# Kernel tuning notes

Hardware: AMD Instinct MI355X
Metric: run time of the kernel (lower is better)

## Reference

```python
import jax, jax.numpy as jnp
import numpy as np


def setup_inputs() -> dict:
    key = jax.random.key(0)
    ks = jax.random.split(key, 4)
    B, H, W, C = 4, 64, 64, 256
    d = C // 8
    x = jax.random.normal(ks[0], (B, H, W, C), dtype=jnp.float32)
    # 1x1 conv weights as [C_in, C_out] matrices (Glorot-ish scale)
    Wq = jax.random.normal(ks[1], (C, d), dtype=jnp.float32) * (1.0 / np.sqrt(C))
    Wk = jax.random.normal(ks[2], (C, d), dtype=jnp.float32) * (1.0 / np.sqrt(C))
    Wv = jax.random.normal(ks[3], (C, C), dtype=jnp.float32) * (1.0 / np.sqrt(C))
    bq = jnp.zeros((d,), dtype=jnp.float32)
    bk = jnp.zeros((d,), dtype=jnp.float32)
    bv = jnp.zeros((C,), dtype=jnp.float32)
    gamma = jnp.float32(0.0)  # matches tf.Variable(0.0)
    return {"x": x, "Wq": Wq, "bq": bq, "Wk": Wk, "bk": bk, "Wv": Wv, "bv": bv, "gamma": gamma}


def reference(x, Wq, bq, Wk, bk, Wv, bv, gamma):
    B, H, W, C = x.shape
    N = H * W
    xf = x.reshape(B, N, C)  # spatial tokens
    q = xf @ Wq + bq  # [B, N, d]
    k = xf @ Wk + bk  # [B, N, d]
    v = xf @ Wv + bv  # [B, N, C]
    energy = jnp.einsum("bnd,bmd->bnm", q, k)  # [B, N, N]
    attn = jax.nn.softmax(energy, axis=-1)
    out = jnp.einsum("bnm,bmc->bnc", attn, v).reshape(B, H, W, C)
    return gamma * out + x
```

## Files before the change

### kernel.cpp

```cpp
#include <hip/hip_runtime.h>
#include <hip/hip_bf16.h>

typedef __attribute__((ext_vector_type(8)))  short short8;
typedef __attribute__((ext_vector_type(4)))  float f32x4;
typedef __attribute__((ext_vector_type(16))) float f32x16;
typedef __attribute__((ext_vector_type(4)))  unsigned int u32x4;

#define LOG2E 1.4426950408889634f

static __device__ __forceinline__ unsigned short f2bf(float f) {
    union { float f; unsigned u; } v; v.f = f;
    unsigned r = v.u + 0x7fffu + ((v.u >> 16) & 1u);
    return (unsigned short)(r >> 16);
}
static __device__ __forceinline__ unsigned cvt_pk_bf16(float lo, float hi) {
    unsigned r;
    asm("v_cvt_pk_bf16_f32 %0, %1, %2" : "=v"(r) : "v"(lo), "v"(hi));
    return r;
}
static __device__ __forceinline__ float exp2_hw(float x) {
    float r;
    asm("v_exp_f32 %0, %1" : "=v"(r) : "v"(x));
    return r;
}

__global__ __launch_bounds__(64) void transpose_w(
    const float* __restrict__ Wq, const float* __restrict__ Wk,
    const float* __restrict__ Wv, unsigned short* __restrict__ Wtf)
{
    const int g  = blockIdx.x;
    const int ct = g >> 3, kk = g & 7;
    const int l  = threadIdx.x;
    const int col = ct * 16 + (l & 15);
    const int k0  = kk * 32 + (l >> 4) * 8;
    const float* W; int c, ldw;
    if (col < 32)      { W = Wq; c = col;      ldw = 32;  }
    else if (col < 64) { W = Wk; c = col - 32; ldw = 32;  }
    else               { W = Wv; c = col - 64; ldw = 256; }
    ushort4 o0, o1;
    o0.x = f2bf(W[(size_t)(k0 + 0) * ldw + c]);
    o0.y = f2bf(W[(size_t)(k0 + 1) * ldw + c]);
    o0.z = f2bf(W[(size_t)(k0 + 2) * ldw + c]);
    o0.w = f2bf(W[(size_t)(k0 + 3) * ldw + c]);
    o1.x = f2bf(W[(size_t)(k0 + 4) * ldw + c]);
    o1.y = f2bf(W[(size_t)(k0 + 5) * ldw + c]);
    o1.z = f2bf(W[(size_t)(k0 + 6) * ldw + c]);
    o1.w = f2bf(W[(size_t)(k0 + 7) * ldw + c]);
    *reinterpret_cast<ushort4*>(Wtf + (size_t)g * 512 + l * 8)     = o0;
    *reinterpret_cast<ushort4*>(Wtf + (size_t)g * 512 + l * 8 + 4) = o1;
}

__global__ __launch_bounds__(256) void proj_kernel(
    const float* __restrict__ x, const unsigned short* __restrict__ Wtf,
    const float* __restrict__ bq, const float* __restrict__ bk,
    const float* __restrict__ bv,
    unsigned short* __restrict__ Qb, unsigned short* __restrict__ Kf,
    unsigned short* __restrict__ Vf)
{
    __shared__ unsigned short x_lds[64][264];
    const int tid = threadIdx.x;
    const int M0  = (blockIdx.x >> 1) * 64;
    const int ctb = (blockIdx.x & 1) * 10;

    #pragma unroll
    for (int j = 0; j < 16; ++j) {
        int idx = j * 256 + tid;
        int row = idx >> 6;
        int qc  = idx & 63;
        const float4 v = *reinterpret_cast<const float4*>(x + (size_t)(M0 + row) * 256 + qc * 4);
        ushort4 o;
        o.x = f2bf(v.x); o.y = f2bf(v.y); o.z = f2bf(v.z); o.w = f2bf(v.w);
        *reinterpret_cast<ushort4*>(&x_lds[row][qc * 4]) = o;
    }
    __syncthreads();

    const int w  = tid >> 6;
    const int l  = tid & 63;
    const int lr = l & 15;
    const int lg = l >> 4;

    short8 a[8];
    #pragma unroll
    for (int kk = 0; kk < 8; ++kk)
        a[kk] = *reinterpret_cast<const short8*>(&x_lds[w * 16 + lr][kk * 32 + lg * 8]);

    const int b   = M0 >> 12;
    const int kt  = (M0 & 4095) >> 6;

    for (int ct = ctb; ct < ctb + 10; ++ct) {
        const int col = ct * 16 + lr;
        f32x4 acc = {0.f, 0.f, 0.f, 0.f};
        #pragma unroll
        for (int kk = 0; kk < 8; ++kk) {
            const short8 bfr = *reinterpret_cast<const short8*>(
                Wtf + ((size_t)ct * 8 + kk) * 512 + l * 8);
            acc = __builtin_amdgcn_mfma_f32_16x16x32_bf16(a[kk], bfr, acc, 0, 0, 0);
        }
        const int rbase = M0 + w * 16 + lg * 4;
        if (ct < 2) {
            const float bias = bq[col];
            #pragma unroll
            for (int r = 0; r < 4; ++r)
                Qb[(size_t)(rbase + r) * 32 + col] = f2bf((acc[r] + bias) * LOG2E);
        } else if (ct < 4) {
            const int colp = col - 32;
            const float bias = bk[colp];
            const int dd = colp >> 4, hj = (colp >> 3) & 1, jj = colp & 7;
            #pragma unroll
            for (int r = 0; r < 4; ++r) {
                const int tt = (rbase + r) & 4095;
                const size_t e = (size_t)b * 131072 + (size_t)kt * 2048
                               + (((tt >> 5) & 1) * 2 + dd) * 512
                               + (hj * 32 + (tt & 31)) * 8 + jj;
                Kf[e] = f2bf(acc[r] + bias);
            }
        } else {
            const int colp = col - 64;
            const float bias = bv[colp];
            const int kk_f = w;
            const int hi_v = (lg >> 1) & 1;
            const int j0   = (lg & 1) * 4;
            const size_t e = (size_t)b * 1048576 + (size_t)kt * 16384
                           + (colp >> 5) * 2048 + kk_f * 512
                           + (hi_v * 32 + (colp & 31)) * 8 + j0;
            ushort4 o;
            o.x = f2bf(acc[0] + bias); o.y = f2bf(acc[1] + bias);
            o.z = f2bf(acc[2] + bias); o.w = f2bf(acc[3] + bias);
            *reinterpret_cast<ushort4*>(Vf + e) = o;
        }
    }
}

__global__ __launch_bounds__(128, 2) void attn_kernel(
    const unsigned short* __restrict__ Qb, const unsigned short* __restrict__ Kf,
    const unsigned short* __restrict__ Vf, const float* __restrict__ x,
    const float* __restrict__ gamma_p, float* __restrict__ out)
{
    __shared__ float O_sh[4][16][64];
    __shared__ float l_sh[2][32];

    const int i  = blockIdx.x;
    const int b  = (i & 7) >> 1;
    const int t  = ((i >> 3) << 1) | (i & 1);
    const int qt = t >> 1;
    const int cg = t & 1;

    const int tid = threadIdx.x;
    const int kh  = tid >> 6;
    const int l   = tid & 63;
    const int l5  = l & 31;
    const int hi  = l >> 5;

    const size_t bN = (size_t)b * 4096;
    const int q0 = qt * 32;
    const int c0 = cg * 128;

    const unsigned short* Kfb = Kf + (size_t)b * 131072 + l * 8;
    const unsigned short* Vfb = Vf + (size_t)b * 1048576 + (c0 >> 5) * 2048 + l * 8;

    short8 qb[2];
    #pragma unroll
    for (int dd = 0; dd < 2; ++dd)
        qb[dd] = *reinterpret_cast<const short8*>(
            Qb + (bN + (size_t)(q0 + l5)) * 32 + dd * 16 + hi * 8);

    f32x16 Oa[4];
    #pragma unroll
    for (int ct = 0; ct < 4; ++ct)
        #pragma unroll
        for (int r = 0; r < 16; ++r) Oa[ct][r] = 0.f;
    float lsum0 = 0.f, lsum1 = 0.f;

    f32x16 z;
    #pragma unroll
    for (int r = 0; r < 16; ++r) z[r] = 0.f;

    const int kt0 = kh * 32;

    auto loadK = [&](short8 (&kA)[2][2], int ktg) {
        const unsigned short* kp = Kfb + (size_t)ktg * 2048;
        #pragma unroll
        for (int ks = 0; ks < 2; ++ks)
            #pragma unroll
            for (int dd = 0; dd < 2; ++dd)
                kA[ks][dd] = *reinterpret_cast<const short8*>(kp + (ks * 2 + dd) * 512);
    };

    auto body = [&](short8 (&kcur)[2][2], short8 (&knxt)[2][2], int ktg, int ktgn) {
        const unsigned short* vp = Vfb + (size_t)ktg * 16384;
        short8 vf[4][4];
        #pragma unroll
        for (int ct = 0; ct < 4; ++ct)
            #pragma unroll
            for (int kk = 0; kk < 4; ++kk)
                vf[ct][kk] = *reinterpret_cast<const short8*>(vp + ct * 2048 + kk * 512);
        loadK(knxt, ktgn);
        f32x16 p0 = __builtin_amdgcn_mfma_f32_32x32x16_bf16(kcur[0][0], qb[0], z, 0, 0, 0);
        p0        = __builtin_amdgcn_mfma_f32_32x32x16_bf16(kcur[0][1], qb[1], p0, 0, 0, 0);
        f32x16 p1 = __builtin_amdgcn_mfma_f32_32x32x16_bf16(kcur[1][0], qb[0], z, 0, 0, 0);
        p1        = __builtin_amdgcn_mfma_f32_32x32x16_bf16(kcur[1][1], qb[1], p1, 0, 0, 0);
        short8 pa[4];
        #pragma unroll
        for (int ks = 0; ks < 2; ++ks) {
            float e[16];
            #pragma unroll
            for (int r = 0; r < 16; ++r) {
                const float s = (ks == 0) ? p0[r] : p1[r];
                e[r] = exp2_hw(s);
                if (r & 1) lsum1 += e[r]; else lsum0 += e[r];
            }
            unsigned c[8];
            #pragma unroll
            for (int n = 0; n < 8; ++n) c[n] = cvt_pk_bf16(e[2 * n], e[2 * n + 1]);
            #pragma unroll
            for (int k2 = 0; k2 < 2; ++k2) {
                unsigned d0 = c[4 * k2 + 0], d2 = c[4 * k2 + 2];
                unsigned d1 = c[4 * k2 + 1], d3 = c[4 * k2 + 3];
                asm("v_permlane32_swap_b32 %0, %1" : "+v"(d0), "+v"(d2));
                asm("v_permlane32_swap_b32 %0, %1" : "+v"(d1), "+v"(d3));
                u32x4 u = {d0, d1, d2, d3};
                pa[ks * 2 + k2] = __builtin_bit_cast(short8, u);
            }
        }
        #pragma unroll
        for (int ct = 0; ct < 4; ++ct)
            #pragma unroll
            for (int kk = 0; kk < 4; ++kk)
                Oa[ct] = __builtin_amdgcn_mfma_f32_32x32x16_bf16(pa[kk], vf[ct][kk], Oa[ct], 0, 0, 0);
    };

    short8 kA0[2][2], kA1[2][2];
    loadK(kA0, kt0);
    for (int kt = 0; kt < 32; kt += 2) {
        body(kA0, kA1, kt0 + kt, kt0 + kt + 1);
        body(kA1, kA0, kt0 + kt + 1, kt0 + ((kt + 2) & 31));
    }

    float lsum = lsum0 + lsum1;
    lsum += __shfl_xor(lsum, 32);
    if (hi == 0) l_sh[kh][l5] = lsum;
    #pragma unroll
    for (int ct = 0; ct < 4; ++ct)
        if ((ct >> 1) != kh) {
            #pragma unroll
            for (int r = 0; r < 16; ++r)
                O_sh[ct][r][hi * 32 + l5] = Oa[ct][r];
        }
    __syncthreads();

    const float gamma = gamma_p[0];
    #pragma unroll
    for (int ct = 0; ct < 4; ++ct)
        if ((ct >> 1) == kh) {
            #pragma unroll
            for (int r = 0; r < 16; ++r) {
                const int qr = (r & 3) + 8 * (r >> 2) + 4 * hi;
                const float ltot = l_sh[0][qr] + l_sh[1][qr];
                const float osum = Oa[ct][r] + O_sh[ct][r][hi * 32 + l5];
                const size_t idx = (bN + (size_t)(q0 + qr)) * 256 + c0 + ct * 32 + l5;
                out[idx] = gamma * (osum / ltot) + x[idx];
            }
        }
}

extern "C" void kernel_launch(void* const* d_in, const int* in_sizes, int n_in,
                              void* d_out, int out_size, void* d_ws, size_t ws_size,
                              hipStream_t stream) {
    const float* x     = (const float*)d_in[0];
    const float* Wq    = (const float*)d_in[1];
    const float* bq    = (const float*)d_in[2];
    const float* Wk    = (const float*)d_in[3];
    const float* bk    = (const float*)d_in[4];
    const float* Wv    = (const float*)d_in[5];
    const float* bv    = (const float*)d_in[6];
    const float* gamma = (const float*)d_in[7];
    float* out = (float*)d_out;

    unsigned short* Qb  = (unsigned short*)d_ws;
    unsigned short* Kf  = Qb + (size_t)16384 * 32;
    unsigned short* Vf  = Kf + (size_t)16384 * 32;
    unsigned short* Wtf = Vf + (size_t)4 * 256 * 4096;

    transpose_w<<<160, 64, 0, stream>>>(Wq, Wk, Wv, Wtf);
    proj_kernel<<<512, 256, 0, stream>>>(x, Wtf, bq, bk, bv, Qb, Kf, Vf);
    attn_kernel<<<1024, 128, 0, stream>>>(Qb, Kf, Vf, x, gamma, out);
}
```

Before: 80.51 us.

## Split attention work by query and channel halves instead of key halves

The attention kernel changes from 2-wave blocks that split the key range, reducing partial outputs through shared memory, to 4-wave blocks. Each wave now owns 32 queries by 64 channels across all keys. This removes the LDS reduction, the block barrier and half of the output accumulators, which lowers register pressure. In exchange, every wave recomputes QK^T scores and exponentials for only 64 channels, doubling the softmax and exp work relative to the useful PV MFMAs.

```diff
diff --git a/kernel.cpp b/kernel.cpp
--- a/kernel.cpp
+++ b/kernel.cpp
@@ -131,13 +131,12 @@
     }
 }
 
-__global__ __launch_bounds__(128, 2) void attn_kernel(
+__global__ __launch_bounds__(256, 2) void attn_kernel(
     const unsigned short* __restrict__ Qb, const unsigned short* __restrict__ Kf,
     const unsigned short* __restrict__ Vf, const float* __restrict__ x,
     const float* __restrict__ gamma_p, float* __restrict__ out)
 {
-    __shared__ float O_sh[4][16][64];
-    __shared__ float l_sh[2][32];
+    __shared__ float l_sh[4][32];
 
     const int i  = blockIdx.x;
     const int b  = (i & 7) >> 1;
@@ -146,14 +145,16 @@
     const int cg = t & 1;
 
     const int tid = threadIdx.x;
-    const int kh  = tid >> 6;
+    const int w   = tid >> 6;
+    const int qh  = w >> 1;
+    const int cs  = w & 1;
     const int l   = tid & 63;
     const int l5  = l & 31;
     const int hi  = l >> 5;
 
     const size_t bN = (size_t)b * 4096;
-    const int q0 = qt * 32;
-    const int c0 = cg * 128;
+    const int q0 = qt * 64 + qh * 32;
+    const int c0 = cg * 128 + cs * 64;
 
     const unsigned short* Kfb = Kf + (size_t)b * 131072 + l * 8;
     const unsigned short* Vfb = Vf + (size_t)b * 1048576 + (c0 >> 5) * 2048 + l * 8;
@@ -164,9 +165,9 @@
         qb[dd] = *reinterpret_cast<const short8*>(
             Qb + (bN + (size_t)(q0 + l5)) * 32 + dd * 16 + hi * 8);
 
-    f32x16 Oa[4];
-    #pragma unroll
-    for (int ct = 0; ct < 4; ++ct)
+    f32x16 Oa[2];
+    #pragma unroll
+    for (int ct = 0; ct < 2; ++ct)
         #pragma unroll
         for (int r = 0; r < 16; ++r) Oa[ct][r] = 0.f;
     float lsum0 = 0.f, lsum1 = 0.f;
@@ -174,8 +175,6 @@
     f32x16 z;
     #pragma unroll
     for (int r = 0; r < 16; ++r) z[r] = 0.f;
-
-    const int kt0 = kh * 32;
 
     auto loadK = [&](short8 (&kA)[2][2], int ktg) {
         const unsigned short* kp = Kfb + (size_t)ktg * 2048;
@@ -188,9 +187,9 @@
 
     auto body = [&](short8 (&kcur)[2][2], short8 (&knxt)[2][2], int ktg, int ktgn) {
         const unsigned short* vp = Vfb + (size_t)ktg * 16384;
-        short8 vf[4][4];
-        #pragma unroll
-        for (int ct = 0; ct < 4; ++ct)
+        short8 vf[2][4];
+        #pragma unroll
+        for (int ct = 0; ct < 2; ++ct)
             #pragma unroll
             for (int kk = 0; kk < 4; ++kk)
                 vf[ct][kk] = *reinterpret_cast<const short8*>(vp + ct * 2048 + kk * 512);
@@ -223,43 +222,32 @@
             }
         }
         #pragma unroll
-        for (int ct = 0; ct < 4; ++ct)
+        for (int ct = 0; ct < 2; ++ct)
             #pragma unroll
             for (int kk = 0; kk < 4; ++kk)
                 Oa[ct] = __builtin_amdgcn_mfma_f32_32x32x16_bf16(pa[kk], vf[ct][kk], Oa[ct], 0, 0, 0);
     };
 
     short8 kA0[2][2], kA1[2][2];
-    loadK(kA0, kt0);
-    for (int kt = 0; kt < 32; kt += 2) {
-        body(kA0, kA1, kt0 + kt, kt0 + kt + 1);
-        body(kA1, kA0, kt0 + kt + 1, kt0 + ((kt + 2) & 31));
+    loadK(kA0, 0);
+    for (int kt = 0; kt < 64; kt += 2) {
+        body(kA0, kA1, kt, kt + 1);
+        body(kA1, kA0, kt + 1, (kt + 2) & 63);
     }
 
     float lsum = lsum0 + lsum1;
     lsum += __shfl_xor(lsum, 32);
-    if (hi == 0) l_sh[kh][l5] = lsum;
-    #pragma unroll
-    for (int ct = 0; ct < 4; ++ct)
-        if ((ct >> 1) != kh) {
-            #pragma unroll
-            for (int r = 0; r < 16; ++r)
-                O_sh[ct][r][hi * 32 + l5] = Oa[ct][r];
-        }
-    __syncthreads();
+    if (hi == 0) l_sh[w][l5] = lsum;
 
     const float gamma = gamma_p[0];
     #pragma unroll
-    for (int ct = 0; ct < 4; ++ct)
-        if ((ct >> 1) == kh) {
-            #pragma unroll
-            for (int r = 0; r < 16; ++r) {
-                const int qr = (r & 3) + 8 * (r >> 2) + 4 * hi;
-                const float ltot = l_sh[0][qr] + l_sh[1][qr];
-                const float osum = Oa[ct][r] + O_sh[ct][r][hi * 32 + l5];
-                const size_t idx = (bN + (size_t)(q0 + qr)) * 256 + c0 + ct * 32 + l5;
-                out[idx] = gamma * (osum / ltot) + x[idx];
-            }
+    for (int ct = 0; ct < 2; ++ct)
+        #pragma unroll
+        for (int r = 0; r < 16; ++r) {
+            const int qr = (r & 3) + 8 * (r >> 2) + 4 * hi;
+            const float ltot = l_sh[w][qr];
+            const size_t idx = (bN + (size_t)(q0 + qr)) * 256 + c0 + ct * 32 + l5;
+            out[idx] = gamma * (Oa[ct][r] / ltot) + x[idx];
         }
 }
 
@@ -283,5 +271,5 @@
 
     transpose_w<<<160, 64, 0, stream>>>(Wq, Wk, Wv, Wtf);
     proj_kernel<<<512, 256, 0, stream>>>(x, Wtf, bq, bk, bv, Qb, Kf, Vf);
-    attn_kernel<<<1024, 128, 0, stream>>>(Qb, Kf, Vf, x, gamma, out);
-}
+    attn_kernel<<<512, 256, 0, stream>>>(Qb, Kf, Vf, x, gamma, out);
+}
```

Result: slower. 180.0 us (+123.5%).
